# Kernel tuning notes

Hardware: AMD Instinct MI355X
Metric: run time of the kernel (lower is better)

## Reference

```python
import jax, jax.numpy as jnp
import numpy as np


def setup_inputs() -> dict:
    key = jax.random.key(0)
    ks = jax.random.split(key, 6)
    N, D_IN, H, DH, N_ITEM = 4096, 512, 8, 128, 256
    x = jax.random.normal(ks[0], (N, D_IN), dtype=jnp.float32)
    y = jax.random.normal(ks[1], (N, D_IN), dtype=jnp.float32)
    # linear1/linear2 have NonNeg kernel constraint -> nonnegative weights
    W1 = jax.random.uniform(ks[2], (D_IN, H * DH), dtype=jnp.float32) * 0.05
    W2 = jax.random.uniform(ks[3], (D_IN, H * DH), dtype=jnp.float32) * 0.05
    W3 = jax.random.normal(ks[4], (D_IN, H * DH), dtype=jnp.float32) * 0.05
    # 1x1 conv with 1 output filter over the head axis == weighted sum over heads
    conv_w = jax.random.normal(ks[5], (H,), dtype=jnp.float32)
    return {"x": x, "y": y, "W1": W1, "W2": W2, "W3": W3,
            "conv_w": conv_w, "nItem": N_ITEM}


def reference(x, y, W1, W2, W3, conv_w, nItem):
    N = x.shape[0]
    H = conv_w.shape[0]
    Dh = W1.shape[1] // H
    nSet = N // nItem
    inv_sqrt = 1.0 / jnp.sqrt(jnp.asarray(Dh, dtype=x.dtype))

    q = (x @ W1).reshape(N, H, Dh).transpose(1, 0, 2)   # [H, N, Dh]
    k = (y @ W2).reshape(N, H, Dh).transpose(1, 0, 2)   # [H, N, Dh]
    v = (y @ W3).reshape(N, H, Dh).transpose(1, 0, 2)   # [H, N, Dh]

    # Full cross-set scores, as in the original: [H, N, N]
    scores = jnp.einsum('hnd,hmd->hnm', q, k) * inv_sqrt

    # Block-diagonal y2 matmul == per-set segmented matmul:
    # newx[h, n, s*Dh:(s+1)*Dh] = scores[h, n, s*nItem:(s+1)*nItem] @ v_set_s
    scores_s = scores.reshape(H, N, nSet, nItem)
    v_s = v.reshape(H, nSet, nItem, Dh)
    newx = jnp.einsum('hnsi,hsid->hnsd', scores_s, v_s) / nItem  # [H, N, nSet, Dh]

    # 1x1 conv mixing heads (single output filter, no bias)
    mixed = jnp.einsum('hnsd,h->nsd', newx, conv_w)  # [N, nSet, Dh]

    # isOnlySelf=False branch: reshape [N, nSet*Dh] -> [N, nSet, Dh]
    return mixed
```

## Files before the change

kernel.cpp:

```cpp
#include <hip/hip_runtime.h>
#include <stdint.h>
#include <stddef.h>


typedef short short8 __attribute__((ext_vector_type(8)));
typedef float f32x4 __attribute__((ext_vector_type(4)));

#define AS1 __attribute__((address_space(1)))
#define AS3 __attribute__((address_space(3)))

__device__ __forceinline__ void gl_lds16(const void* g, void* l) {
    __builtin_amdgcn_global_load_lds((AS1 void*)(uintptr_t)g, (AS3 void*)l, 16, 0, 0);
}

__device__ __forceinline__ short f2bf(float f) {
    union { float f; unsigned u; } v; v.f = f;
    unsigned r = v.u + 0x7FFFu + ((v.u >> 16) & 1u);
    return (short)(r >> 16);
}

__global__ __launch_bounds__(256)
void prep(const float* __restrict__ x, const float* __restrict__ y,
          const float* __restrict__ W1, const float* __restrict__ W2,
          const float* __restrict__ W3, short* __restrict__ xb,
          short* __restrict__ yb, short* __restrict__ w1b,
          short* __restrict__ w23t) {
    const int b = blockIdx.x, tid = threadIdx.x;
    if (b < 2048) {
        const float* in = (b < 1024) ? x : y;
        short* o = (b < 1024) ? xb : yb;
        const int i = (b & 1023) * 256 + tid;
        const float4* p = (const float4*)in + (size_t)i * 2;
        float4 a = p[0], c4 = p[1];
        short8 s8;
        s8[0] = f2bf(a.x);  s8[1] = f2bf(a.y);
        s8[2] = f2bf(a.z);  s8[3] = f2bf(a.w);
        s8[4] = f2bf(c4.x); s8[5] = f2bf(c4.y);
        s8[6] = f2bf(c4.z); s8[7] = f2bf(c4.w);
        *((short8*)o + i) = s8;
        return;
    }
    if (b >= 3072) {
        const int i = (b - 3072) * 256 + tid;
        const float4* p = (const float4*)W1 + (size_t)i * 2;
        float4 a = p[0], c4 = p[1];
        short8 s8;
        s8[0] = f2bf(a.x);  s8[1] = f2bf(a.y);
        s8[2] = f2bf(a.z);  s8[3] = f2bf(a.w);
        s8[4] = f2bf(c4.x); s8[5] = f2bf(c4.y);
        s8[6] = f2bf(c4.z); s8[7] = f2bf(c4.w);
        *((short8*)w1b + i) = s8;
        return;
    }
    __shared__ float t[32][33];
    const int b2 = b - 2048;
    const int z = b2 >> 9;
    const float* W = z ? W3 : W2;
    short* Wt = w23t + (size_t)z * 1024 * 512;
    const int b3 = b2 & 511;
    const int bx = (b3 & 31) * 32, by = (b3 >> 5) * 32;
    const int tx = tid & 31, ty = tid >> 5;
    #pragma unroll
    for (int j = 0; j < 4; ++j)
        t[ty + j * 8][tx] = W[(size_t)(by + ty + j * 8) * 1024 + bx + tx];
    __syncthreads();
    #pragma unroll
    for (int j = 0; j < 4; ++j)
        Wt[(size_t)(bx + ty + j * 8) * 512 + by + tx] = f2bf(t[tx][ty + j * 8]);
}

template <int OUTMODE>
__device__ __forceinline__
void gemm_tile(const short* __restrict__ A, int lda,
               const short* __restrict__ Bt, int ldb,
               void* __restrict__ Cout, int ldc, int K,
               int bx, int by, float scale, char* smem) {
    const int tid = threadIdx.x;
    const int wave = tid >> 6, lane = tid & 63;
    const int quad = lane >> 4, ml = lane & 15;
    const int m0 = by * 128, n0 = bx * 128;
    const int wm0 = (wave >> 1) * 64, wn0 = (wave & 1) * 64;
    const int srow = lane >> 2, skoff = (lane & 3) * 8;

    f32x4 acc[4][4];
    #pragma unroll
    for (int i = 0; i < 4; ++i)
        #pragma unroll
        for (int j = 0; j < 4; ++j) {
            acc[i][j][0] = 0.f; acc[i][j][1] = 0.f;
            acc[i][j][2] = 0.f; acc[i][j][3] = 0.f;
        }

    auto STAGE = [&](char* sbuf, int kt) {
        #pragma unroll
        for (int ci = 0; ci < 4; ++ci) {
            const int c = wave + ci * 4;
            if (c < 8)
                gl_lds16(A + (size_t)(m0 + c * 16 + srow) * lda + kt + skoff,
                         sbuf + c * 1024 + lane * 16);
            else
                gl_lds16(Bt + (size_t)(n0 + (c - 8) * 16 + srow) * ldb + kt + skoff,
                         sbuf + 8192 + (c - 8) * 1024 + lane * 16);
        }
    };

    const int nt = K >> 5;
    STAGE(smem, 0);
    __syncthreads();

    int cur = 0;
    for (int t = 0; t < nt; ++t) {
        char* sbuf = smem + cur * 16384;
        if (t + 1 < nt)
            STAGE(smem + (cur ^ 1) * 16384, (t + 1) * 32);

        const short* sA = (const short*)sbuf;
        const short* sB = (const short*)(sbuf + 8192);
        short8 af[4], bfr[4];
        #pragma unroll
        for (int mt = 0; mt < 4; ++mt)
            af[mt] = *(const short8*)(sA + (wm0 + mt * 16 + ml) * 32 + quad * 8);
        #pragma unroll
        for (int nt2 = 0; nt2 < 4; ++nt2)
            bfr[nt2] = *(const short8*)(sB + (wn0 + nt2 * 16 + ml) * 32 + quad * 8);

        #pragma unroll
        for (int mt = 0; mt < 4; ++mt)
            #pragma unroll
            for (int nt2 = 0; nt2 < 4; ++nt2)
                acc[mt][nt2] = __builtin_amdgcn_mfma_f32_16x16x32_bf16(
                    af[mt], bfr[nt2], acc[mt][nt2], 0, 0, 0);

        __syncthreads();
        cur ^= 1;
    }

    #pragma unroll
    for (int mt = 0; mt < 4; ++mt)
        #pragma unroll
        for (int nt2 = 0; nt2 < 4; ++nt2) {
            const int col = n0 + wn0 + nt2 * 16 + ml;
            #pragma unroll
            for (int r = 0; r < 4; ++r) {
                const int row = m0 + wm0 + mt * 16 + quad * 4 + r;
                float v = acc[mt][nt2][r];
                if (OUTMODE == 2) v *= scale;
                if (OUTMODE == 0)
                    ((float*)Cout)[(size_t)row * ldc + col] = v;
                else
                    ((short*)Cout)[(size_t)row * ldc + col] = f2bf(v);
            }
        }
}

__global__ __launch_bounds__(256)
void stage_kv(const short* __restrict__ yb, const short* __restrict__ w23t,
              short* __restrict__ kvt) {
    __shared__ char smem[32768];
    const int b = blockIdx.x;
    gemm_tile<1>(w23t, 512, yb, 512, kvt, 4096, 512,
                 b & 31, b >> 5, 1.f, smem);
}

__global__ __launch_bounds__(256)
void build_u(const short* __restrict__ kvt, const float* __restrict__ cw,
             short* __restrict__ Ut) {
    __shared__ char smem[32768];
    const int s = blockIdx.x, h = blockIdx.y;
    const float scale = cw[h] * (0.08838834764831845f / 256.0f);
    gemm_tile<2>(kvt + (size_t)(1024 + h * 128) * 4096 + s * 256, 4096,
                 kvt + (size_t)(h * 128) * 4096 + s * 256, 4096,
                 Ut + (size_t)(s * 128) * 1024 + h * 128, 1024, 256,
                 0, 0, scale, smem);
}

__global__ __launch_bounds__(256)
void build_m(const short* __restrict__ Ut, const short* __restrict__ w1b,
             short* __restrict__ M) {
    __shared__ char smem[32768];
    gemm_tile<1>(Ut, 1024, w1b, 1024, M, 512, 1024,
                 blockIdx.x, blockIdx.y, 1.f, smem);
}

__global__ __launch_bounds__(256)
void gemm_out(const short* __restrict__ xb, const short* __restrict__ M,
              float* __restrict__ out) {
    __shared__ char smem[32768];
    gemm_tile<0>(xb, 512, M, 512, out, 2048, 512,
                 blockIdx.x, blockIdx.y, 1.f, smem);
}

extern "C" void kernel_launch(void* const* d_in, const int* in_sizes, int n_in,
                              void* d_out, int out_size, void* d_ws, size_t ws_size,
                              hipStream_t stream) {
    const float* x  = (const float*)d_in[0];
    const float* y  = (const float*)d_in[1];
    const float* W1 = (const float*)d_in[2];
    const float* W2 = (const float*)d_in[3];
    const float* W3 = (const float*)d_in[4];
    const float* cw = (const float*)d_in[5];
    float* out = (float*)d_out;

    short* xb   = (short*)d_ws;
    short* yb   = xb   + (size_t)4096 * 512;
    short* w23t = yb   + (size_t)4096 * 512;
    short* w1b  = w23t + (size_t)2048 * 512;
    short* kvt  = w1b  + (size_t)512 * 1024;
    short* Ut   = kvt  + (size_t)2048 * 4096;
    short* M    = Ut   + (size_t)2048 * 1024;

    prep<<<3328, 256, 0, stream>>>(x, y, W1, W2, W3, xb, yb, w1b, w23t);
    stage_kv<<<512, 256, 0, stream>>>(yb, w23t, kvt);
    build_u<<<dim3(16, 8), 256, 0, stream>>>(kvt, cw, Ut);
    build_m<<<dim3(4, 16), 256, 0, stream>>>(Ut, w1b, M);
    gemm_out<<<dim3(16, 32), 256, 0, stream>>>(xb, M, out);
}
```

Baseline: 138.6 us.

## Deepen GEMM K-tile to 64 with XOR-swizzled LDS and XCD-aware block mapping

The shared GEMM tile now stages 64-wide K slices instead of 32, halving the number of barrier iterations. It XOR-swizzles the 16-byte chunks in LDS so the MFMA fragment reads avoid bank conflicts. The large kernels remap block indices so neighbouring tiles land on the same XCD, improving L2 reuse. LDS per block doubles to 64KB, which can reduce occupancy.

New measurement: 129.4 us. 1.07x faster.

```diff
diff --git a/kernel.cpp b/kernel.cpp
--- a/kernel.cpp
+++ b/kernel.cpp
@@ -80,7 +80,9 @@
     const int quad = lane >> 4, ml = lane & 15;
     const int m0 = by * 128, n0 = bx * 128;
     const int wm0 = (wave >> 1) * 64, wn0 = (wave & 1) * 64;
-    const int srow = lane >> 2, skoff = (lane & 3) * 8;
+    const int rl = lane >> 3;
+    const int ch = lane & 7;
+    const int sch = ch ^ rl;
 
     f32x4 acc[4][4];
     #pragma unroll
@@ -93,46 +95,53 @@
 
     auto STAGE = [&](char* sbuf, int kt) {
         #pragma unroll
-        for (int ci = 0; ci < 4; ++ci) {
-            const int c = wave + ci * 4;
-            if (c < 8)
-                gl_lds16(A + (size_t)(m0 + c * 16 + srow) * lda + kt + skoff,
-                         sbuf + c * 1024 + lane * 16);
-            else
-                gl_lds16(Bt + (size_t)(n0 + (c - 8) * 16 + srow) * ldb + kt + skoff,
-                         sbuf + 8192 + (c - 8) * 1024 + lane * 16);
+        for (int j = 0; j < 4; ++j) {
+            const int r = (wave * 4 + j) * 8 + rl;
+            gl_lds16(A + (size_t)(m0 + r) * lda + kt + sch * 8,
+                     sbuf + (wave * 4 + j) * 1024 + lane * 16);
+        }
+        #pragma unroll
+        for (int j = 0; j < 4; ++j) {
+            const int r = (wave * 4 + j) * 8 + rl;
+            gl_lds16(Bt + (size_t)(n0 + r) * ldb + kt + sch * 8,
+                     sbuf + 16384 + (wave * 4 + j) * 1024 + lane * 16);
         }
     };
 
-    const int nt = K >> 5;
+    const int nt = K >> 6;
     STAGE(smem, 0);
     __syncthreads();
 
-    int cur = 0;
     for (int t = 0; t < nt; ++t) {
-        char* sbuf = smem + cur * 16384;
+        char* sbuf = smem + (t & 1) * 32768;
         if (t + 1 < nt)
-            STAGE(smem + (cur ^ 1) * 16384, (t + 1) * 32);
+            STAGE(smem + ((t + 1) & 1) * 32768, (t + 1) * 64);
 
         const short* sA = (const short*)sbuf;
-        const short* sB = (const short*)(sbuf + 8192);
-        short8 af[4], bfr[4];
-        #pragma unroll
-        for (int mt = 0; mt < 4; ++mt)
-            af[mt] = *(const short8*)(sA + (wm0 + mt * 16 + ml) * 32 + quad * 8);
-        #pragma unroll
-        for (int nt2 = 0; nt2 < 4; ++nt2)
-            bfr[nt2] = *(const short8*)(sB + (wn0 + nt2 * 16 + ml) * 32 + quad * 8);
-
-        #pragma unroll
-        for (int mt = 0; mt < 4; ++mt)
-            #pragma unroll
-            for (int nt2 = 0; nt2 < 4; ++nt2)
-                acc[mt][nt2] = __builtin_amdgcn_mfma_f32_16x16x32_bf16(
-                    af[mt], bfr[nt2], acc[mt][nt2], 0, 0, 0);
-
+        const short* sB = (const short*)(sbuf + 16384);
+        #pragma unroll
+        for (int kk = 0; kk < 2; ++kk) {
+            short8 af[4], bfr[4];
+            #pragma unroll
+            for (int mt = 0; mt < 4; ++mt) {
+                const int row = wm0 + mt * 16 + ml;
+                af[mt] = *(const short8*)(sA + row * 64 +
+                                          (((kk << 2) + quad) ^ (row & 7)) * 8);
+            }
+            #pragma unroll
+            for (int nt2 = 0; nt2 < 4; ++nt2) {
+                const int row = wn0 + nt2 * 16 + ml;
+                bfr[nt2] = *(const short8*)(sB + row * 64 +
+                                            (((kk << 2) + quad) ^ (row & 7)) * 8);
+            }
+            #pragma unroll
+            for (int mt = 0; mt < 4; ++mt)
+                #pragma unroll
+                for (int nt2 = 0; nt2 < 4; ++nt2)
+                    acc[mt][nt2] = __builtin_amdgcn_mfma_f32_16x16x32_bf16(
+                        af[mt], bfr[nt2], acc[mt][nt2], 0, 0, 0);
+        }
         __syncthreads();
-        cur ^= 1;
     }
 
     #pragma unroll
@@ -153,11 +162,15 @@
         }
 }
 
+__device__ __forceinline__ int xcd_swz512(int b) {
+    return (b & 7) * 64 + (b >> 3);
+}
+
 __global__ __launch_bounds__(256)
 void stage_kv(const short* __restrict__ yb, const short* __restrict__ w23t,
               short* __restrict__ kvt) {
-    __shared__ char smem[32768];
-    const int b = blockIdx.x;
+    __shared__ char smem[65536];
+    const int b = xcd_swz512(blockIdx.x);
     gemm_tile<1>(w23t, 512, yb, 512, kvt, 4096, 512,
                  b & 31, b >> 5, 1.f, smem);
 }
@@ -165,7 +178,7 @@
 __global__ __launch_bounds__(256)
 void build_u(const short* __restrict__ kvt, const float* __restrict__ cw,
              short* __restrict__ Ut) {
-    __shared__ char smem[32768];
+    __shared__ char smem[65536];
     const int s = blockIdx.x, h = blockIdx.y;
     const float scale = cw[h] * (0.08838834764831845f / 256.0f);
     gemm_tile<2>(kvt + (size_t)(1024 + h * 128) * 4096 + s * 256, 4096,
@@ -177,7 +190,7 @@
 __global__ __launch_bounds__(256)
 void build_m(const short* __restrict__ Ut, const short* __restrict__ w1b,
              short* __restrict__ M) {
-    __shared__ char smem[32768];
+    __shared__ char smem[65536];
     gemm_tile<1>(Ut, 1024, w1b, 1024, M, 512, 1024,
                  blockIdx.x, blockIdx.y, 1.f, smem);
 }
@@ -185,9 +198,10 @@
 __global__ __launch_bounds__(256)
 void gemm_out(const short* __restrict__ xb, const short* __restrict__ M,
               float* __restrict__ out) {
-    __shared__ char smem[32768];
+    __shared__ char smem[65536];
+    const int b = xcd_swz512(blockIdx.x);
     gemm_tile<0>(xb, 512, M, 512, out, 2048, 512,
-                 blockIdx.x, blockIdx.y, 1.f, smem);
+                 b & 15, b >> 4, 1.f, smem);
 }
 
 extern "C" void kernel_launch(void* const* d_in, const int* in_sizes, int n_in,
@@ -213,5 +227,5 @@
     stage_kv<<<512, 256, 0, stream>>>(yb, w23t, kvt);
     build_u<<<dim3(16, 8), 256, 0, stream>>>(kvt, cw, Ut);
     build_m<<<dim3(4, 16), 256, 0, stream>>>(Ut, w1b, M);
-    gemm_out<<<dim3(16, 32), 256, 0, stream>>>(xb, M, out);
-}
+    gemm_out<<<512, 256, 0, stream>>>(xb, M, out);
+}
```
